# Performance work log

Hardware: AMD Instinct MI355X
Metric: run time of the kernel (lower is better)

Reference implementation:

```python
import jax, jax.numpy as jnp
import numpy as np

B, T, D = 4, 4096, 1024
H, HD = 16, 64
EPS = 1e-6


def setup_inputs() -> dict:
    key = jax.random.key(0)
    ks = jax.random.split(key, 5)
    scale = 1.0 / np.sqrt(D)
    return {
        "x": jax.random.normal(ks[0], (B, T, D), dtype=jnp.float32),
        "Wq": jax.random.normal(ks[1], (D, H * HD), dtype=jnp.float32) * scale,
        "Wk": jax.random.normal(ks[2], (D, H * HD), dtype=jnp.float32) * scale,
        "Wv": jax.random.normal(ks[3], (D, H * HD), dtype=jnp.float32) * scale,
        "Wo": jax.random.normal(ks[4], (H * HD, D), dtype=jnp.float32) * scale,
    }


def _feature_map(x):
    # ELU + 1 feature map (always positive)
    return jax.nn.elu(x) + 1.0


def _causal_linear_attention(q, k, v, eps=EPS):
    # q,k,v: (B,H,T,Dk/Dv) -> scan over T with running state
    Dk = q.shape[-1]
    Dv = v.shape[-1]
    qT = jnp.moveaxis(q, 2, 0)  # (T,B,H,Dk)
    kT = jnp.moveaxis(k, 2, 0)
    vT = jnp.moveaxis(v, 2, 0)

    S0 = jnp.zeros((q.shape[0], q.shape[1], Dk, Dv), dtype=q.dtype)
    z0 = jnp.zeros((q.shape[0], q.shape[1], Dk), dtype=q.dtype)

    def step(carry, qkv_t):
        S, z = carry
        q_t, k_t, v_t = qkv_t
        S = S + jnp.einsum('bhd,bhe->bhde', k_t, v_t)
        z = z + k_t
        num = jnp.einsum('bhd,bhde->bhe', q_t, S)
        den = jnp.einsum('bhd,bhd->bh', q_t, z) + eps
        return (S, z), num / den[..., None]

    _, yT = jax.lax.scan(step, (S0, z0), (qT, kT, vT))  # yT: (T,B,H,Dv)
    return jnp.moveaxis(yT, 0, 2)  # (B,H,T,Dv)


def reference(x, Wq, Wk, Wv, Wo):
    b, t, _ = x.shape

    def proj(W):
        return (x @ W).reshape(b, t, H, HD).transpose(0, 2, 1, 3)  # (B,H,T,HD)

    q = _feature_map(proj(Wq))
    k = _feature_map(proj(Wk))
    v = proj(Wv)
    y = _causal_linear_attention(q, k, v)  # (B,H,T,HD)
    y = y.transpose(0, 2, 1, 3).reshape(b, t, H * HD)
    return y @ Wo
```

## Files before the change

### kernel.cpp

```cpp
#include <hip/hip_runtime.h>


typedef __bf16 bf16;
typedef __bf16 bf16x8 __attribute__((ext_vector_type(8)));
typedef float f32x4 __attribute__((ext_vector_type(4)));

#define EPS 1e-6f

__device__ __forceinline__ void gl_lds16(const void* g, void* l) {
  __builtin_amdgcn_global_load_lds(
      (__attribute__((address_space(1))) void*)g,
      (__attribute__((address_space(3))) void*)l, 16, 0, 0);
}

__device__ __forceinline__ float fmact(float v) {
  return v > 0.f ? v + 1.f : __expf(v);
}

__global__ __launch_bounds__(256) void cvt_bf16(const float* __restrict__ in,
                                                bf16* __restrict__ out, int n8) {
  int i = blockIdx.x * 256 + threadIdx.x;
  if (i >= n8) return;
  size_t base = (size_t)i * 8;
  float4 v0 = *(const float4*)&in[base];
  float4 v1 = *(const float4*)&in[base + 4];
  bf16x8 o;
  o[0] = (bf16)v0.x; o[1] = (bf16)v0.y; o[2] = (bf16)v0.z; o[3] = (bf16)v0.w;
  o[4] = (bf16)v1.x; o[5] = (bf16)v1.y; o[6] = (bf16)v1.z; o[7] = (bf16)v1.w;
  *(bf16x8*)&out[base] = o;
}

__global__ __launch_bounds__(256) void wtrans(const float* __restrict__ W,
                                              bf16* __restrict__ WT) {
  __shared__ float tile[64][65];
  const int k0 = blockIdx.x * 64, n0 = blockIdx.y * 64;
  const int t = threadIdx.x;
  {
    const int r4 = t / 16, c4 = (t % 16) * 4;
#pragma unroll
    for (int rr = 0; rr < 4; ++rr) {
      int r = r4 + rr * 16;
      float4 v = *(const float4*)&W[(size_t)(k0 + r) * 1024 + n0 + c4];
      tile[r][c4] = v.x; tile[r][c4 + 1] = v.y;
      tile[r][c4 + 2] = v.z; tile[r][c4 + 3] = v.w;
    }
  }
  __syncthreads();
  const int nl = t / 4, kb = (t % 4) * 16;
  bf16x8 o0, o1;
#pragma unroll
  for (int j = 0; j < 8; ++j) {
    o0[j] = (bf16)tile[kb + j][nl];
    o1[j] = (bf16)tile[kb + 8 + j][nl];
  }
  *(bf16x8*)&WT[(size_t)(n0 + nl) * 1024 + k0 + kb] = o0;
  *(bf16x8*)&WT[(size_t)(n0 + nl) * 1024 + k0 + kb + 8] = o1;
}

template <int PROJ>
__global__ __launch_bounds__(256) void gemm_bt(const bf16* __restrict__ A,
                                               const bf16* __restrict__ BT,
                                               bf16* __restrict__ Obf,
                                               float* __restrict__ Of, int N) {
  __shared__ alignas(16) bf16 As[128 * 32];
  __shared__ alignas(16) bf16 Bs[128 * 32];
  const int t = threadIdx.x;
  const int m0 = blockIdx.x * 128, n0 = blockIdx.y * 128;
  const int l = t & 63, w = t >> 6;
  const int wm = (w >> 1) * 64, wn = (w & 1) * 64;
  const int lr = l & 15, lg = l >> 4, lk = lg * 8;
  f32x4 acc[4][4] = {};
  const int ar = t >> 2;
  const int ac = (t & 3) * 8;
  bf16* asw = As + w * 512;
  bf16* bsw = Bs + w * 512;
  const bf16* pa0 = A + (size_t)(m0 + ar) * 1024 + ac;
  const bf16* pa1 = A + (size_t)(m0 + ar + 64) * 1024 + ac;
  const bf16* pb0 = BT + (size_t)(n0 + ar) * 1024 + ac;
  const bf16* pb1 = BT + (size_t)(n0 + ar + 64) * 1024 + ac;
  for (int k0 = 0; k0 < 1024; k0 += 32) {
    gl_lds16(pa0 + k0, asw);
    gl_lds16(pa1 + k0, asw + 2048);
    gl_lds16(pb0 + k0, bsw);
    gl_lds16(pb1 + k0, bsw + 2048);
    __syncthreads();
    bf16x8 af[4], bfv[4];
#pragma unroll
    for (int m = 0; m < 4; ++m)
      af[m] = *(const bf16x8*)&As[(wm + m * 16 + lr) * 32 + lk];
#pragma unroll
    for (int n = 0; n < 4; ++n)
      bfv[n] = *(const bf16x8*)&Bs[(wn + n * 16 + lr) * 32 + lk];
#pragma unroll
    for (int m = 0; m < 4; ++m)
#pragma unroll
      for (int n = 0; n < 4; ++n)
        acc[m][n] = __builtin_amdgcn_mfma_f32_16x16x32_bf16(af[m], bfv[n],
                                                            acc[m][n], 0, 0, 0);
    __syncthreads();
  }
  const size_t ldo = (size_t)N;
#pragma unroll
  for (int m = 0; m < 4; ++m)
#pragma unroll
    for (int n = 0; n < 4; ++n)
#pragma unroll
      for (int r = 0; r < 4; ++r) {
        int row = m0 + wm + m * 16 + lg * 4 + r;
        int col = n0 + wn + n * 16 + lr;
        float v = acc[m][n][r];
        if (PROJ) {
          if (col < 2048) v = fmact(v);
          Obf[(size_t)row * ldo + col] = (bf16)v;
        } else {
          Of[(size_t)row * ldo + col] = v;
        }
      }
}

__global__ __launch_bounds__(256) void chunk_ktv(const bf16* __restrict__ QKV,
                                                 float* __restrict__ S_ws,
                                                 float* __restrict__ z_ws) {
  const int blk = blockIdx.x;
  const int bh = blk >> 5, c = blk & 31;
  const int b = bh >> 4, h = bh & 15;
  const size_t rowbase = (size_t)b * 4096 + (size_t)c * 128;
  __shared__ alignas(16) bf16 KT[64 * 136];
  __shared__ alignas(16) bf16 VT[64 * 136];
  const int t = threadIdx.x;
  {
    const int r = t >> 1, c0 = (t & 1) * 32;
    const bf16* kp = QKV + (rowbase + r) * 3072 + 1024 + h * 64 + c0;
    const bf16* vp = QKV + (rowbase + r) * 3072 + 2048 + h * 64 + c0;
    bf16x8 kv[4], vv[4];
#pragma unroll
    for (int q8 = 0; q8 < 4; ++q8) {
      kv[q8] = *(const bf16x8*)&kp[q8 * 8];
      vv[q8] = *(const bf16x8*)&vp[q8 * 8];
    }
#pragma unroll
    for (int q8 = 0; q8 < 4; ++q8)
#pragma unroll
      for (int j = 0; j < 8; ++j) {
        KT[(c0 + q8 * 8 + j) * 136 + r] = kv[q8][j];
        VT[(c0 + q8 * 8 + j) * 136 + r] = vv[q8][j];
      }
  }
  __syncthreads();
  if (t < 64) {
    float z = 0.f;
    for (int tt = 0; tt < 128; ++tt) z += (float)KT[t * 136 + tt];
    z_ws[(size_t)blk * 64 + t] = z;
  }
  const int l = t & 63, w = t >> 6;
  const int lr = l & 15, lg = l >> 4, lk = lg * 8;
  f32x4 acc[4] = {};
#pragma unroll
  for (int ks = 0; ks < 4; ++ks) {
    const int k0 = ks * 32;
    bf16x8 a = *(const bf16x8*)&KT[(w * 16 + lr) * 136 + k0 + lk];
#pragma unroll
    for (int n = 0; n < 4; ++n) {
      bf16x8 bv = *(const bf16x8*)&VT[(n * 16 + lr) * 136 + k0 + lk];
      acc[n] = __builtin_amdgcn_mfma_f32_16x16x32_bf16(a, bv, acc[n], 0, 0, 0);
    }
  }
#pragma unroll
  for (int n = 0; n < 4; ++n)
#pragma unroll
    for (int r = 0; r < 4; ++r) {
      int d = w * 16 + lg * 4 + r;
      int e = n * 16 + lr;
      S_ws[((size_t)blk * 64 + d) * 64 + e] = acc[n][r];
    }
}

__global__ __launch_bounds__(256) void prefix_scan(const float* __restrict__ S_ws,
                                                   const float* __restrict__ z_ws,
                                                   bf16* __restrict__ STp,
                                                   float* __restrict__ zP) {
  const int bh = blockIdx.x;
  const int t = threadIdx.x;
  __shared__ float sbuf[4096];
  float racc[16];
#pragma unroll
  for (int u = 0; u < 16; ++u) racc[u] = 0.f;
  const int e = t >> 2, d0 = (t & 3) * 16;
  float zr = 0.f;
  for (int c = 0; c < 32; ++c) {
    const size_t cb = (size_t)bh * 32 + c;
    bf16x8 o0, o1;
#pragma unroll
    for (int u = 0; u < 8; ++u) {
      o0[u] = (bf16)racc[u];
      o1[u] = (bf16)racc[8 + u];
    }
    *(bf16x8*)&STp[cb * 4096 + e * 64 + d0] = o0;
    *(bf16x8*)&STp[cb * 4096 + e * 64 + d0 + 8] = o1;
    if (t < 64) {
      zP[cb * 64 + t] = zr;
      zr += z_ws[cb * 64 + t];
    }
    const float* Sc = S_ws + cb * 4096;
#pragma unroll
    for (int q4 = 0; q4 < 4; ++q4)
      *(float4*)&sbuf[t * 16 + q4 * 4] = *(const float4*)&Sc[t * 16 + q4 * 4];
    __syncthreads();
#pragma unroll
    for (int u = 0; u < 16; ++u) racc[u] += sbuf[(d0 + u) * 64 + e];
    __syncthreads();
  }
}

__global__ __launch_bounds__(256) void chunk_attn(const bf16* __restrict__ QKV,
                                                  const bf16* __restrict__ STp,
                                                  const float* __restrict__ zP,
                                                  bf16* __restrict__ Y) {
  const int blk = blockIdx.x;
  const int bh = blk >> 5, c = blk & 31;
  const int b = bh >> 4, h = bh & 15;
  const size_t cb = (size_t)bh * 32 + c;
  const size_t rowbase = (size_t)b * 4096 + (size_t)c * 128;
  const bf16* Q = QKV + rowbase * 3072 + h * 64;
  const bf16* K = QKV + rowbase * 3072 + 1024 + h * 64;
  const bf16* V = QKV + rowbase * 3072 + 2048 + h * 64;
  __shared__ alignas(16) bf16 VT[64 * 136];
  __shared__ alignas(16) bf16 P[128 * 136];
  __shared__ float den[128];
  const int t = threadIdx.x;
  {
    const int r = t >> 1, c0 = (t & 1) * 32;
    const bf16* vp = V + (size_t)r * 3072 + c0;
    bf16x8 vv[4];
#pragma unroll
    for (int q8 = 0; q8 < 4; ++q8) vv[q8] = *(const bf16x8*)&vp[q8 * 8];
#pragma unroll
    for (int q8 = 0; q8 < 4; ++q8)
#pragma unroll
      for (int j = 0; j < 8; ++j) VT[(c0 + q8 * 8 + j) * 136 + r] = vv[q8][j];
  }
  const int l = t & 63, w = t >> 6;
  const int lr = l & 15, lg = l >> 4, lk = lg * 8;
  f32x4 acc[2][4] = {};
  f32x4 accs[2][8] = {};
#pragma unroll
  for (int kq = 0; kq < 2; ++kq) {
    const int k0 = kq * 32;
    bf16x8 am[2];
#pragma unroll
    for (int m = 0; m < 2; ++m)
      am[m] = *(const bf16x8*)&Q[(size_t)(w * 32 + m * 16 + lr) * 3072 + k0 + lk];
#pragma unroll
    for (int n = 0; n < 4; ++n) {
      bf16x8 bs = *(const bf16x8*)&STp[cb * 4096 + (size_t)(n * 16 + lr) * 64 + k0 + lk];
#pragma unroll
      for (int m = 0; m < 2; ++m)
        acc[m][n] = __builtin_amdgcn_mfma_f32_16x16x32_bf16(am[m], bs, acc[m][n], 0, 0, 0);
    }
#pragma unroll
    for (int n = 0; n < 8; ++n) {
      bf16x8 bk = *(const bf16x8*)&K[(size_t)(n * 16 + lr) * 3072 + k0 + lk];
#pragma unroll
      for (int m = 0; m < 2; ++m)
        accs[m][n] = __builtin_amdgcn_mfma_f32_16x16x32_bf16(am[m], bk, accs[m][n], 0, 0, 0);
    }
  }
#pragma unroll
  for (int m = 0; m < 2; ++m)
#pragma unroll
    for (int r = 0; r < 4; ++r) {
      const int row_c = w * 32 + m * 16 + lg * 4 + r;
      float s = 0.f;
#pragma unroll
      for (int n = 0; n < 8; ++n) {
        const int col_c = n * 16 + lr;
        float v = accs[m][n][r];
        v = (col_c <= row_c) ? v : 0.f;
        accs[m][n][r] = v;
        s += v;
      }
      s += __shfl_xor(s, 1);
      s += __shfl_xor(s, 2);
      s += __shfl_xor(s, 4);
      s += __shfl_xor(s, 8);
      if (lr == 0) den[row_c] = s;
#pragma unroll
      for (int n = 0; n < 8; ++n)
        P[row_c * 136 + n * 16 + lr] = (bf16)accs[m][n][r];
    }
  __syncthreads();
  if (t < 128) {
    float s = EPS;
    const bf16* qr = Q + (size_t)t * 3072;
    const float* zp = zP + cb * 64;
#pragma unroll
    for (int d8 = 0; d8 < 64; d8 += 8) {
      bf16x8 qv = *(const bf16x8*)&qr[d8];
#pragma unroll
      for (int j = 0; j < 8; ++j) s += (float)qv[j] * zp[d8 + j];
    }
    den[t] += s;
  }
#pragma unroll
  for (int ks = 0; ks < 4; ++ks) {
    const int k0 = ks * 32;
    bf16x8 ap[2];
#pragma unroll
    for (int m = 0; m < 2; ++m)
      ap[m] = *(const bf16x8*)&P[(w * 32 + m * 16 + lr) * 136 + k0 + lk];
#pragma unroll
    for (int n = 0; n < 4; ++n) {
      bf16x8 bv = *(const bf16x8*)&VT[(n * 16 + lr) * 136 + k0 + lk];
#pragma unroll
      for (int m = 0; m < 2; ++m)
        acc[m][n] = __builtin_amdgcn_mfma_f32_16x16x32_bf16(ap[m], bv, acc[m][n], 0, 0, 0);
    }
  }
  __syncthreads();
#pragma unroll
  for (int m = 0; m < 2; ++m)
#pragma unroll
    for (int n = 0; n < 4; ++n)
#pragma unroll
      for (int r = 0; r < 4; ++r) {
        const int row_c = w * 32 + m * 16 + lg * 4 + r;
        const int col = n * 16 + lr;
        float y = acc[m][n][r] / den[row_c];
        Y[(rowbase + row_c) * 1024 + h * 64 + col] = (bf16)y;
      }
}

extern "C" void kernel_launch(void* const* d_in, const int* in_sizes, int n_in,
                              void* d_out, int out_size, void* d_ws, size_t ws_size,
                              hipStream_t stream) {
  (void)in_sizes; (void)n_in; (void)out_size; (void)ws_size;
  const float* x  = (const float*)d_in[0];
  const float* Wq = (const float*)d_in[1];
  const float* Wk = (const float*)d_in[2];
  const float* Wv = (const float*)d_in[3];
  const float* Wo = (const float*)d_in[4];
  char* ws = (char*)d_ws;
  bf16*  XB   = (bf16*)ws;
  bf16*  WT3  = (bf16*)(ws + 33554432);
  bf16*  WOT  = (bf16*)(ws + 39845888);
  bf16*  QKV  = (bf16*)(ws + 41943040);
  float* S_ws = (float*)(ws + 142606336);
  float* z_ws = (float*)(ws + 176160768);
  bf16*  STp  = (bf16*)(ws + 176685056);
  float* zP   = (float*)(ws + 193462272);
  bf16*  Y    = XB;

  cvt_bf16<<<8192, 256, 0, stream>>>(x, XB, 2097152);
  wtrans<<<dim3(16, 16), 256, 0, stream>>>(Wq, WT3);
  wtrans<<<dim3(16, 16), 256, 0, stream>>>(Wk, WT3 + 1048576);
  wtrans<<<dim3(16, 16), 256, 0, stream>>>(Wv, WT3 + 2097152);
  wtrans<<<dim3(16, 16), 256, 0, stream>>>(Wo, WOT);
  gemm_bt<1><<<dim3(128, 24), 256, 0, stream>>>(XB, WT3, QKV, nullptr, 3072);
  chunk_ktv<<<2048, 256, 0, stream>>>(QKV, S_ws, z_ws);
  prefix_scan<<<64, 256, 0, stream>>>(S_ws, z_ws, STp, zP);
  chunk_attn<<<2048, 256, 0, stream>>>(QKV, STp, zP, Y);
  gemm_bt<0><<<dim3(128, 8), 256, 0, stream>>>(Y, WOT, nullptr, (float*)d_out, 1024);
}
```

Baseline: 322.7 us.

## Replace GEMMs with 256x256 pipelined 8-wave kernel and parallelize prefix scan

Both projection GEMMs move from a 128x128 tile, 4-wave, single-buffered kernel to a 256x256 tile, 8-wave kernel. The new kernel double-buffers LDS with an XOR swizzle, uses manual vmcnt waits and barriers, raises wave priority around the MFMA blocks, and remaps workgroups across XCDs. chunk_ktv now writes S transposed, so prefix_scan can read rows directly without an LDS transpose or barriers, and the scan is split across 4x more blocks. The intent is to cut GEMM memory stalls and the serial scan latency, at the cost of 128KB dynamic LDS, hand-written synchronization, and register pressure.

```diff
diff --git a/kernel.cpp b/kernel.cpp
--- a/kernel.cpp
+++ b/kernel.cpp
@@ -2,10 +2,15 @@
 
 
 typedef __bf16 bf16;
+typedef __bf16 bf16x4 __attribute__((ext_vector_type(4)));
 typedef __bf16 bf16x8 __attribute__((ext_vector_type(8)));
 typedef float f32x4 __attribute__((ext_vector_type(4)));
 
 #define EPS 1e-6f
+
+#define BAR() asm volatile("s_barrier" ::: "memory")
+#define VMCNT4() asm volatile("s_waitcnt vmcnt(4)" ::: "memory")
+#define VMCNT0() asm volatile("s_waitcnt vmcnt(0)" ::: "memory")
 
 __device__ __forceinline__ void gl_lds16(const void* g, void* l) {
   __builtin_amdgcn_global_load_lds(
@@ -58,50 +63,92 @@
 }
 
 template <int PROJ>
-__global__ __launch_bounds__(256) void gemm_bt(const bf16* __restrict__ A,
-                                               const bf16* __restrict__ BT,
-                                               bf16* __restrict__ Obf,
-                                               float* __restrict__ Of, int N) {
-  __shared__ alignas(16) bf16 As[128 * 32];
-  __shared__ alignas(16) bf16 Bs[128 * 32];
+__global__ __launch_bounds__(512, 2) void gemm8(const bf16* __restrict__ A,
+                                                const bf16* __restrict__ BT,
+                                                bf16* __restrict__ Obf,
+                                                float* __restrict__ Of,
+                                                const int N, const int gy) {
+  extern __shared__ bf16 lds[];
   const int t = threadIdx.x;
-  const int m0 = blockIdx.x * 128, n0 = blockIdx.y * 128;
-  const int l = t & 63, w = t >> 6;
-  const int wm = (w >> 1) * 64, wn = (w & 1) * 64;
-  const int lr = l & 15, lg = l >> 4, lk = lg * 8;
-  f32x4 acc[4][4] = {};
-  const int ar = t >> 2;
-  const int ac = (t & 3) * 8;
-  bf16* asw = As + w * 512;
-  bf16* bsw = Bs + w * 512;
-  const bf16* pa0 = A + (size_t)(m0 + ar) * 1024 + ac;
-  const bf16* pa1 = A + (size_t)(m0 + ar + 64) * 1024 + ac;
-  const bf16* pb0 = BT + (size_t)(n0 + ar) * 1024 + ac;
-  const bf16* pb1 = BT + (size_t)(n0 + ar + 64) * 1024 + ac;
-  for (int k0 = 0; k0 < 1024; k0 += 32) {
-    gl_lds16(pa0 + k0, asw);
-    gl_lds16(pa1 + k0, asw + 2048);
-    gl_lds16(pb0 + k0, bsw);
-    gl_lds16(pb1 + k0, bsw + 2048);
-    __syncthreads();
-    bf16x8 af[4], bfv[4];
-#pragma unroll
-    for (int m = 0; m < 4; ++m)
-      af[m] = *(const bf16x8*)&As[(wm + m * 16 + lr) * 32 + lk];
-#pragma unroll
-    for (int n = 0; n < 4; ++n)
-      bfv[n] = *(const bf16x8*)&Bs[(wn + n * 16 + lr) * 32 + lk];
-#pragma unroll
-    for (int m = 0; m < 4; ++m)
-#pragma unroll
-      for (int n = 0; n < 4; ++n)
-        acc[m][n] = __builtin_amdgcn_mfma_f32_16x16x32_bf16(af[m], bfv[n],
-                                                            acc[m][n], 0, 0, 0);
-    __syncthreads();
-  }
-  const size_t ldo = (size_t)N;
-#pragma unroll
-  for (int m = 0; m < 4; ++m)
+  const int w = t >> 6, l = t & 63;
+  const int nwg = (int)gridDim.x, cpx = nwg >> 3;
+  const int f = ((int)blockIdx.x & 7) * cpx + ((int)blockIdx.x >> 3);
+  const int bx = f / gy, by = f - bx * gy;
+  const int m0 = bx * 256, n0 = by * 256;
+  const int wm = (w >> 2) * 128, wn = (w & 3) * 64;
+  const int lr = l & 15, lg = l >> 4;
+  const int aslc = (w >> 2) * 8192;
+  const int bslc = 16384 + ((w & 3) >> 1) * 8192;
+  const int brow = (w & 1) * 64;
+  const int srow = t >> 3;
+  const int scol = ((t & 7) ^ (((t >> 5) & 1) << 1)) * 8;
+
+  f32x4 acc[8][4] = {};
+  bf16x8 bv[8];
+
+#define FRAG(c, slc, sr_, ks_)                                          \
+  (*(const bf16x8*)&lds[(c) * 32768 + (slc) + (sr_) * 64 +              \
+                        (((ks_) * 32 + lg * 8) ^ (((sr_) & 4) << 2))])
+
+#define STG(dbuf, slc, rbase, PTR, kt)                                        \
+  do {                                                                        \
+    const bf16* _s = (PTR) + (size_t)((rbase) + srow) * 1024 + (kt) * 64 + scol; \
+    bf16* _d = lds + (dbuf) * 32768 + (slc) + w * 512;                        \
+    gl_lds16(_s, _d);                                                         \
+    gl_lds16(_s + 65536, _d + 4096);                                          \
+  } while (0)
+
+#define PHASE(c, q, STAGE_STMT, VM)                                           \
+  {                                                                           \
+    bf16x8 av[4];                                                             \
+    _Pragma("unroll") for (int mi = 0; mi < 2; ++mi)                          \
+      _Pragma("unroll") for (int kk = 0; kk < 2; ++kk)                        \
+        av[mi * 2 + kk] = FRAG(c, aslc, (q) * 32 + mi * 16 + lr, kk);         \
+    if ((q) == 0) {                                                           \
+      _Pragma("unroll") for (int n = 0; n < 4; ++n)                           \
+        _Pragma("unroll") for (int kk = 0; kk < 2; ++kk)                      \
+          bv[n * 2 + kk] = FRAG(c, bslc, brow + n * 16 + lr, kk);             \
+    }                                                                         \
+    STAGE_STMT;                                                               \
+    if (VM) VMCNT4();                                                         \
+    BAR();                                                                    \
+    __builtin_amdgcn_s_setprio(1);                                            \
+    _Pragma("unroll") for (int mi = 0; mi < 2; ++mi)                          \
+      _Pragma("unroll") for (int n = 0; n < 4; ++n)                           \
+        _Pragma("unroll") for (int kk = 0; kk < 2; ++kk)                      \
+          acc[(q) * 2 + mi][n] = __builtin_amdgcn_mfma_f32_16x16x32_bf16(     \
+              av[mi * 2 + kk], bv[n * 2 + kk], acc[(q) * 2 + mi][n], 0, 0, 0);\
+    __builtin_amdgcn_s_setprio(0);                                            \
+    BAR();                                                                    \
+  }
+
+  STG(0, 0, m0, A, 0);        STG(0, 8192, m0 + 128, A, 0);
+  STG(0, 16384, n0, BT, 0);   STG(0, 24576, n0 + 128, BT, 0);
+  STG(1, 16384, n0, BT, 1);   STG(1, 24576, n0 + 128, BT, 1);
+  VMCNT4();
+  BAR();
+
+#pragma unroll 1
+  for (int I = 0; I < 8; ++I) {
+    const int t2 = 2 * I;
+    const int k1 = t2 + 1;
+    const int k2 = (t2 + 2 > 15) ? 15 : t2 + 2;
+    const int k3 = (t2 + 3 > 15) ? 15 : t2 + 3;
+    PHASE(0, 0, STG(1, 0, m0, A, k1), 0);
+    PHASE(0, 1, STG(1, 8192, m0 + 128, A, k1), 0);
+    PHASE(0, 2, STG(0, 16384, n0, BT, k2), 0);
+    PHASE(0, 3, STG(0, 24576, n0 + 128, BT, k2), 1);
+    PHASE(1, 0, STG(0, 0, m0, A, k2), 0);
+    PHASE(1, 1, STG(0, 8192, m0 + 128, A, k2), 0);
+    PHASE(1, 2, STG(1, 16384, n0, BT, k3), 0);
+    PHASE(1, 3, STG(1, 24576, n0 + 128, BT, k3), 1);
+  }
+  VMCNT0();
+#undef PHASE
+#undef STG
+#undef FRAG
+#pragma unroll
+  for (int m = 0; m < 8; ++m)
 #pragma unroll
     for (int n = 0; n < 4; ++n)
 #pragma unroll
@@ -111,9 +158,9 @@
         float v = acc[m][n][r];
         if (PROJ) {
           if (col < 2048) v = fmact(v);
-          Obf[(size_t)row * ldo + col] = (bf16)v;
+          Obf[(size_t)row * N + col] = (bf16)v;
         } else {
-          Of[(size_t)row * ldo + col] = v;
+          Of[(size_t)row * N + col] = v;
         }
       }
 }
@@ -158,20 +205,20 @@
 #pragma unroll
   for (int ks = 0; ks < 4; ++ks) {
     const int k0 = ks * 32;
-    bf16x8 a = *(const bf16x8*)&KT[(w * 16 + lr) * 136 + k0 + lk];
+    bf16x8 a = *(const bf16x8*)&VT[(w * 16 + lr) * 136 + k0 + lk];
 #pragma unroll
     for (int n = 0; n < 4; ++n) {
-      bf16x8 bv = *(const bf16x8*)&VT[(n * 16 + lr) * 136 + k0 + lk];
-      acc[n] = __builtin_amdgcn_mfma_f32_16x16x32_bf16(a, bv, acc[n], 0, 0, 0);
+      bf16x8 bk = *(const bf16x8*)&KT[(n * 16 + lr) * 136 + k0 + lk];
+      acc[n] = __builtin_amdgcn_mfma_f32_16x16x32_bf16(a, bk, acc[n], 0, 0, 0);
     }
   }
 #pragma unroll
   for (int n = 0; n < 4; ++n)
 #pragma unroll
     for (int r = 0; r < 4; ++r) {
-      int d = w * 16 + lg * 4 + r;
-      int e = n * 16 + lr;
-      S_ws[((size_t)blk * 64 + d) * 64 + e] = acc[n][r];
+      int e = w * 16 + lg * 4 + r;
+      int d = n * 16 + lr;
+      S_ws[((size_t)blk * 64 + e) * 64 + d] = acc[n][r];
     }
 }
 
@@ -179,36 +226,22 @@
                                                    const float* __restrict__ z_ws,
                                                    bf16* __restrict__ STp,
                                                    float* __restrict__ zP) {
-  const int bh = blockIdx.x;
+  const int bh = blockIdx.x >> 2, dq = blockIdx.x & 3;
   const int t = threadIdx.x;
-  __shared__ float sbuf[4096];
-  float racc[16];
-#pragma unroll
-  for (int u = 0; u < 16; ++u) racc[u] = 0.f;
-  const int e = t >> 2, d0 = (t & 3) * 16;
-  float zr = 0.f;
+  const int e = t >> 2, d0 = dq * 16 + (t & 3) * 4;
+  float r0 = 0.f, r1 = 0.f, r2 = 0.f, r3 = 0.f, zr = 0.f;
+  const bool doz = (dq == 0) && (t < 64);
   for (int c = 0; c < 32; ++c) {
     const size_t cb = (size_t)bh * 32 + c;
-    bf16x8 o0, o1;
-#pragma unroll
-    for (int u = 0; u < 8; ++u) {
-      o0[u] = (bf16)racc[u];
-      o1[u] = (bf16)racc[8 + u];
-    }
-    *(bf16x8*)&STp[cb * 4096 + e * 64 + d0] = o0;
-    *(bf16x8*)&STp[cb * 4096 + e * 64 + d0 + 8] = o1;
-    if (t < 64) {
+    bf16x4 o;
+    o[0] = (bf16)r0; o[1] = (bf16)r1; o[2] = (bf16)r2; o[3] = (bf16)r3;
+    *(bf16x4*)&STp[cb * 4096 + e * 64 + d0] = o;
+    if (doz) {
       zP[cb * 64 + t] = zr;
       zr += z_ws[cb * 64 + t];
     }
-    const float* Sc = S_ws + cb * 4096;
-#pragma unroll
-    for (int q4 = 0; q4 < 4; ++q4)
-      *(float4*)&sbuf[t * 16 + q4 * 4] = *(const float4*)&Sc[t * 16 + q4 * 4];
-    __syncthreads();
-#pragma unroll
-    for (int u = 0; u < 16; ++u) racc[u] += sbuf[(d0 + u) * 64 + e];
-    __syncthreads();
+    float4 v = *(const float4*)&S_ws[cb * 4096 + e * 64 + d0];
+    r0 += v.x; r1 += v.y; r2 += v.z; r3 += v.w;
   }
 }
 
@@ -350,14 +383,22 @@
   float* zP   = (float*)(ws + 193462272);
   bf16*  Y    = XB;
 
+  {
+    auto k1 = gemm8<1>; auto k0 = gemm8<0>;
+    (void)hipFuncSetAttribute((const void*)k1,
+        hipFuncAttributeMaxDynamicSharedMemorySize, 131072);
+    (void)hipFuncSetAttribute((const void*)k0,
+        hipFuncAttributeMaxDynamicSharedMemorySize, 131072);
+  }
+
   cvt_bf16<<<8192, 256, 0, stream>>>(x, XB, 2097152);
   wtrans<<<dim3(16, 16), 256, 0, stream>>>(Wq, WT3);
   wtrans<<<dim3(16, 16), 256, 0, stream>>>(Wk, WT3 + 1048576);
   wtrans<<<dim3(16, 16), 256, 0, stream>>>(Wv, WT3 + 2097152);
   wtrans<<<dim3(16, 16), 256, 0, stream>>>(Wo, WOT);
-  gemm_bt<1><<<dim3(128, 24), 256, 0, stream>>>(XB, WT3, QKV, nullptr, 3072);
+  gemm8<1><<<768, 512, 131072, stream>>>(XB, WT3, QKV, nullptr, 3072, 12);
   chunk_ktv<<<2048, 256, 0, stream>>>(QKV, S_ws, z_ws);
-  prefix_scan<<<64, 256, 0, stream>>>(S_ws, z_ws, STp, zP);
+  prefix_scan<<<256, 256, 0, stream>>>(S_ws, z_ws, STp, zP);
   chunk_attn<<<2048, 256, 0, stream>>>(QKV, STp, zP, Y);
-  gemm_bt<0><<<dim3(128, 8), 256, 0, stream>>>(Y, WOT, nullptr, (float*)d_out, 1024);
-}
+  gemm8<0><<<256, 512, 131072, stream>>>(Y, WOT, nullptr, (float*)d_out, 1024, 4);
+}
```

Result: faster. 278.5 us (-13.7%).
